# Kernel optimization log

Measured on AMD Instinct MI355X. Metric: run time of the kernel, lower is better.

## Reference

```python
import jax, jax.numpy as jnp
import numpy as np

N, E = 10000, 320000          # nodes, edges
NF, EF = 128, 64              # raw node / edge feat dims
HN, HE = 256, 256             # hidden node / edge dims
NO, EO = 128, 64              # decoder out dims
ITERS = 3


def _w(k, shape):
    # Linear/GRU weight init scaled by fan_in
    return jax.random.normal(k, shape, jnp.float32) / np.sqrt(shape[-1])


def setup_inputs() -> dict:
    key = jax.random.key(0)
    ks = jax.random.split(key, 12)
    return dict(
        nf=jax.random.normal(ks[0], (N, NF), jnp.float32),
        ef=jax.random.normal(ks[1], (E, EF), jnp.float32),
        src=jax.random.randint(ks[2], (E,), 0, N),
        dst=jax.random.randint(ks[3], (E,), 0, N),
        # encoders
        Wne=_w(ks[4], (HN, NF)), bne=jnp.zeros((HN,), jnp.float32),
        Wee=_w(ks[5], (HE, EF)), bee=jnp.zeros((HE,), jnp.float32),
        # edge GRUCell: input = concat(h_src, h_dst) -> 2*HN
        Wih_e=_w(ks[6], (3 * HE, 2 * HN)), Whh_e=_w(ks[7], (3 * HE, HE)),
        bih_e=jnp.zeros((3 * HE,), jnp.float32), bhh_e=jnp.zeros((3 * HE,), jnp.float32),
        # node GRUCell: input = aggregated edge messages -> HE
        Wih_n=_w(ks[8], (3 * HN, HE)), Whh_n=_w(ks[9], (3 * HN, HN)),
        bih_n=jnp.zeros((3 * HN,), jnp.float32), bhh_n=jnp.zeros((3 * HN,), jnp.float32),
        # decoders (MLP with num_neurons=[] == single Linear)
        Wnd=_w(ks[10], (NO, HN)), bnd=jnp.zeros((NO,), jnp.float32),
        Wed=_w(ks[11], (EO, HE)), bed=jnp.zeros((EO,), jnp.float32),
    )


def _gru(x, h, Wih, Whh, bih, bhh):
    # torch.nn.GRUCell math
    gi = x @ Wih.T + bih
    gh = h @ Whh.T + bhh
    ir, iz, inn = jnp.split(gi, 3, axis=-1)
    hr, hz, hn = jnp.split(gh, 3, axis=-1)
    r = jax.nn.sigmoid(ir + hr)
    z = jax.nn.sigmoid(iz + hz)
    n = jnp.tanh(inn + r * hn)
    return (1.0 - z) * n + z * h


def reference(nf, ef, src, dst, Wne, bne, Wee, bee,
              Wih_e, Whh_e, bih_e, bhh_e,
              Wih_n, Whh_n, bih_n, bhh_n,
              Wnd, bnd, Wed, bed):
    # encode
    unf = nf @ Wne.T + bne   # [N, HN]
    uef = ef @ Wee.T + bee   # [E, HE]
    # GRUMPNN: iterative GRU-based message passing
    for _ in range(ITERS):
        xe = jnp.concatenate([unf[src], unf[dst]], axis=-1)      # [E, 2*HN]
        uef = _gru(xe, uef, Wih_e, Whh_e, bih_e, bhh_e)           # edge update
        agg = jax.ops.segment_sum(uef, dst, num_segments=N)       # [N, HE]
        unf = _gru(agg, unf, Wih_n, Whh_n, bih_n, bhh_n)          # node update
    # decode
    return unf @ Wnd.T + bnd, uef @ Wed.T + bed
```

## Files before the change

### kernel.cpp

```cpp
#include <hip/hip_runtime.h>
#include <hip/hip_bf16.h>
#include <cstddef>

typedef _Float16 f16;
typedef f16 f16x8 __attribute__((ext_vector_type(8)));
typedef f16 f16x4 __attribute__((ext_vector_type(4)));
typedef f16 f16x16 __attribute__((ext_vector_type(16)));
typedef float f32x4 __attribute__((ext_vector_type(4)));

#define NNODES 10000
#define NEDGES 320000

__global__ void pack_b(const float* __restrict__ W, f16* __restrict__ P,
                       int Nout, int K, int ldw, int k0) {
    int idx = blockIdx.x * 256 + threadIdx.x;
    int total = Nout * K;
    if (idx >= total) return;
    int i = idx & 7;
    int l = (idx >> 3) & 63;
    int rest = idx >> 9;
    int NB = Nout >> 4;
    int nb = rest % NB;
    int ks = rest / NB;
    int k = ks * 32 + ((l >> 4) << 3) + i;
    int n = nb * 16 + (l & 15);
    P[idx] = (f16)W[(size_t)n * ldw + k0 + k];
}

template <int AMODE, int OMODE>
__global__ void gemm_bias(const void* __restrict__ A_, const f16* __restrict__ P,
                          const float* __restrict__ bias, void* __restrict__ C_,
                          int M, int Nout, int K) {
    const int lane = threadIdx.x & 63, wave = threadIdx.x >> 6;
    const int wm = wave >> 1, wn = wave & 1;
    const int rb = blockIdx.x * 64 + wm * 32;
    const int cb = blockIdx.y * 64 + wn * 32;
    const int NB = Nout >> 4;
    const int kl = (lane >> 4) << 3;
    int r0 = rb + (lane & 15);
    int r1 = r0 + 16;
    int rc0 = r0 < M ? r0 : M - 1;
    int rc1 = r1 < M ? r1 : M - 1;
    f32x4 acc[2][2] = {};
    for (int ks = 0; ks < (K >> 5); ++ks) {
        int kb = ks * 32 + kl;
        f16x8 a0, a1;
        if constexpr (AMODE == 1) {
            const f16* A = (const f16*)A_;
            a0 = *(const f16x8*)(A + (size_t)rc0 * K + kb);
            a1 = *(const f16x8*)(A + (size_t)rc1 * K + kb);
        } else {
            const float* A = (const float*)A_;
            const float* p0 = A + (size_t)rc0 * K + kb;
            const float* p1 = A + (size_t)rc1 * K + kb;
#pragma unroll
            for (int i = 0; i < 8; ++i) { a0[i] = (f16)p0[i]; a1[i] = (f16)p1[i]; }
        }
#pragma unroll
        for (int nf = 0; nf < 2; ++nf) {
            int nb = (cb >> 4) + nf;
            f16x8 b = *(const f16x8*)(P + (((size_t)ks * NB + nb) * 64 + lane) * 8);
            acc[0][nf] = __builtin_amdgcn_mfma_f32_16x16x32_f16(a0, b, acc[0][nf], 0, 0, 0);
            acc[1][nf] = __builtin_amdgcn_mfma_f32_16x16x32_f16(a1, b, acc[1][nf], 0, 0, 0);
        }
    }
#pragma unroll
    for (int mf = 0; mf < 2; ++mf)
#pragma unroll
        for (int nf = 0; nf < 2; ++nf)
#pragma unroll
            for (int reg = 0; reg < 4; ++reg) {
                int row = rb + mf * 16 + ((lane >> 4) << 2) + reg;
                int col = cb + nf * 16 + (lane & 15);
                if (row < M) {
                    float v = acc[mf][nf][reg] + bias[col];
                    if constexpr (OMODE == 0)
                        ((float*)C_)[(size_t)row * Nout + col] = v;
                    else
                        ((f16*)C_)[(size_t)row * Nout + col] = (f16)v;
                }
            }
}

template <bool BIAS>
__global__ void gemm_gi(const f16* __restrict__ A, const f16* __restrict__ P,
                        const float* __restrict__ bias, f16* __restrict__ G, int M) {
    const int lane = threadIdx.x & 63, wave = threadIdx.x >> 6;
    const int wm = wave >> 1, wn = wave & 1;
    const int rb = blockIdx.x * 64 + wm * 32;
    const int cb = blockIdx.y * 64 + wn * 32;
    const int NB = 48;
    const int kl = (lane >> 4) << 3;
    int r0 = rb + (lane & 15);
    int r1 = r0 + 16;
    int rc0 = r0 < M ? r0 : M - 1;
    int rc1 = r1 < M ? r1 : M - 1;
    f32x4 acc[2][2] = {};
    for (int ks = 0; ks < 8; ++ks) {
        int kb = ks * 32 + kl;
        f16x8 a0 = *(const f16x8*)(A + (size_t)rc0 * 256 + kb);
        f16x8 a1 = *(const f16x8*)(A + (size_t)rc1 * 256 + kb);
#pragma unroll
        for (int nf = 0; nf < 2; ++nf) {
            int nb = (cb >> 4) + nf;
            f16x8 b = *(const f16x8*)(P + (((size_t)ks * NB + nb) * 64 + lane) * 8);
            acc[0][nf] = __builtin_amdgcn_mfma_f32_16x16x32_f16(a0, b, acc[0][nf], 0, 0, 0);
            acc[1][nf] = __builtin_amdgcn_mfma_f32_16x16x32_f16(a1, b, acc[1][nf], 0, 0, 0);
        }
    }
#pragma unroll
    for (int mf = 0; mf < 2; ++mf)
#pragma unroll
        for (int nf = 0; nf < 2; ++nf)
#pragma unroll
            for (int reg = 0; reg < 4; ++reg) {
                int row = rb + mf * 16 + ((lane >> 4) << 2) + reg;
                int col = cb + nf * 16 + (lane & 15);
                if (row < M) {
                    float v = acc[mf][nf][reg];
                    if constexpr (BIAS) v += bias[col];
                    G[(size_t)row * 1024 + (col & 255) * 4 + (col >> 8)] = (f16)v;
                }
            }
}

__device__ inline float sigmoidf_(float x) {
    return __fdividef(1.f, 1.f + __expf(-x));
}
__device__ inline float tanhf_(float x) {
    float t = __expf(2.f * x);
    return 1.f - __fdividef(2.f, t + 1.f);
}

__global__ __launch_bounds__(1024, 4) void edge_gru(
        const f16* __restrict__ Gs, const f16* __restrict__ Gd,
        f16* __restrict__ uef,
        const int* __restrict__ src, const int* __restrict__ dst,
        const f16* __restrict__ Phh, const float* __restrict__ bhh) {
    __shared__ int s_idx[128];
    __shared__ char lds_h[64 * 528];
    const int t = threadIdx.x;
    const int e0 = blockIdx.x * 64;
    if (t < 64) s_idx[t] = src[e0 + t];
    else if (t < 128) s_idx[t] = dst[e0 + t - 64];
#pragma unroll
    for (int i = 0; i < 2; ++i) {
        int s = t + i * 1024;
        int row = s >> 5, seg = s & 31;
        f16x8 v = *(const f16x8*)(uef + (size_t)(e0 + row) * 256 + seg * 8);
        *(f16x8*)(lds_h + row * 528 + seg * 16) = v;
    }
    __syncthreads();
    const int lane = t & 63;
    const int wv = t >> 6;
    const int klb = (lane >> 4) << 4;
    const int erow = lane & 15;
    f32x4 acc[3][4] = {};
#pragma unroll
    for (int ks = 0; ks < 8; ++ks) {
        f16x8 b[4];
#pragma unroll
        for (int eg = 0; eg < 4; ++eg)
            b[eg] = *(const f16x8*)(lds_h + (eg * 16 + erow) * 528 + ks * 64 + klb);
#pragma unroll
        for (int g = 0; g < 3; ++g) {
            f16x8 a = *(const f16x8*)(Phh + (size_t)g * 65536
                                      + (((size_t)ks * 16 + wv) * 64 + lane) * 8);
#pragma unroll
            for (int eg = 0; eg < 4; ++eg)
                acc[g][eg] = __builtin_amdgcn_mfma_f32_16x16x32_f16(a, b[eg], acc[g][eg], 0, 0, 0);
        }
    }
    __syncthreads();
    {
        const int j0 = wv * 16 + ((lane >> 4) << 2);
        const f32x4 bhr = *(const f32x4*)(bhh + j0);
        const f32x4 bhz = *(const f32x4*)(bhh + 256 + j0);
        const f32x4 bhn = *(const f32x4*)(bhh + 512 + j0);
#pragma unroll
        for (int eg = 0; eg < 4; ++eg) {
            const int rr = eg * 16 + erow;
            const int sn = s_idx[rr], dn = s_idx[64 + rr];
            f16x16 gsv = *(const f16x16*)(Gs + (size_t)sn * 1024 + j0 * 4);
            f16x16 gdv = *(const f16x16*)(Gd + (size_t)dn * 1024 + j0 * 4);
            f16x4 hv = *(const f16x4*)(lds_h + rr * 528 + j0 * 2);
            f16x4 outv;
#pragma unroll
            for (int q = 0; q < 4; ++q) {
                float ir = (float)gsv[q * 4 + 0] + (float)gdv[q * 4 + 0];
                float iz = (float)gsv[q * 4 + 1] + (float)gdv[q * 4 + 1];
                float in = (float)gsv[q * 4 + 2] + (float)gdv[q * 4 + 2];
                float r = sigmoidf_(ir + acc[0][eg][q] + bhr[q]);
                float z = sigmoidf_(iz + acc[1][eg][q] + bhz[q]);
                float nn = tanhf_(in + r * (acc[2][eg][q] + bhn[q]));
                float h = (float)hv[q];
                outv[q] = (f16)(nn + z * (h - nn));
            }
            *(f16x4*)(lds_h + rr * 528 + j0 * 2) = outv;
        }
    }
    __syncthreads();
#pragma unroll
    for (int i = 0; i < 2; ++i) {
        int s = t + i * 1024;
        int row = s >> 5, seg = s & 31;
        f16x8 v = *(const f16x8*)(lds_h + row * 528 + seg * 16);
        *(f16x8*)(uef + (size_t)(e0 + row) * 256 + seg * 8) = v;
    }
}

__global__ __launch_bounds__(1024) void node_gru(
        const float* __restrict__ agg, f16* __restrict__ unf16,
        const f16* __restrict__ Pih, const f16* __restrict__ Phh,
        const float* __restrict__ bih, const float* __restrict__ bhh, int M) {
    const int lane = threadIdx.x & 63, wave = threadIdx.x >> 6;
    const int wm = wave & 1, wn = wave >> 1;
    const int rb = blockIdx.x * 64 + wm * 32;
    const int cb = wn * 32;
    const int nb0 = wn * 2;
    const int kl = (lane >> 4) << 3;
    int r0 = rb + (lane & 15), r1 = r0 + 16;
    int rc0 = r0 < M ? r0 : M - 1;
    int rc1 = r1 < M ? r1 : M - 1;
    f32x4 acc[4][2][2] = {};
#pragma unroll
    for (int ks = 0; ks < 8; ++ks) {
        const float* p0 = agg + (size_t)rc0 * 256 + ks * 32 + kl;
        const float* p1 = agg + (size_t)rc1 * 256 + ks * 32 + kl;
        f16x8 a0, a1;
#pragma unroll
        for (int i = 0; i < 8; ++i) { a0[i] = (f16)p0[i]; a1[i] = (f16)p1[i]; }
#pragma unroll
        for (int g = 0; g < 3; ++g) {
            const f16* Pg = Pih + (size_t)g * (256 * 256);
#pragma unroll
            for (int nf = 0; nf < 2; ++nf) {
                f16x8 b = *(const f16x8*)(Pg + (((size_t)ks * 16 + nb0 + nf) * 64 + lane) * 8);
                acc[g][0][nf] = __builtin_amdgcn_mfma_f32_16x16x32_f16(a0, b, acc[g][0][nf], 0, 0, 0);
                acc[g][1][nf] = __builtin_amdgcn_mfma_f32_16x16x32_f16(a1, b, acc[g][1][nf], 0, 0, 0);
            }
        }
    }
#pragma unroll
    for (int ks = 0; ks < 8; ++ks) {
        f16x8 a0 = *(const f16x8*)(unf16 + (size_t)rc0 * 256 + ks * 32 + kl);
        f16x8 a1 = *(const f16x8*)(unf16 + (size_t)rc1 * 256 + ks * 32 + kl);
#pragma unroll
        for (int g = 0; g < 3; ++g) {
            const f16* Pg = Phh + (size_t)g * (256 * 256);
            const int tgt = (g == 2) ? 3 : g;
#pragma unroll
            for (int nf = 0; nf < 2; ++nf) {
                f16x8 b = *(const f16x8*)(Pg + (((size_t)ks * 16 + nb0 + nf) * 64 + lane) * 8);
                acc[tgt][0][nf] = __builtin_amdgcn_mfma_f32_16x16x32_f16(a0, b, acc[tgt][0][nf], 0, 0, 0);
                acc[tgt][1][nf] = __builtin_amdgcn_mfma_f32_16x16x32_f16(a1, b, acc[tgt][1][nf], 0, 0, 0);
            }
        }
    }
    __syncthreads();
#pragma unroll
    for (int mf = 0; mf < 2; ++mf) {
        const int row = rb + mf * 16 + ((lane >> 4) << 2);
#pragma unroll
        for (int nf = 0; nf < 2; ++nf) {
            const int j = cb + nf * 16 + (lane & 15);
            const float b_r = bih[j] + bhh[j];
            const float b_z = bih[256 + j] + bhh[256 + j];
            const float b_i = bih[512 + j];
            const float b_h = bhh[512 + j];
#pragma unroll
            for (int reg = 0; reg < 4; ++reg) {
                const int rr = row + reg;
                if (rr < M) {
                    float r = sigmoidf_(acc[0][mf][nf][reg] + b_r);
                    float z = sigmoidf_(acc[1][mf][nf][reg] + b_z);
                    float nn = tanhf_(acc[2][mf][nf][reg] + b_i + r * (acc[3][mf][nf][reg] + b_h));
                    float h = (float)unf16[(size_t)rr * 256 + j];
                    unf16[(size_t)rr * 256 + j] = (f16)(nn + z * (h - nn));
                }
            }
        }
    }
}

__global__ void hist_k(const int* __restrict__ dst, int* __restrict__ cnt, int E) {
    int e = blockIdx.x * 256 + threadIdx.x;
    if (e < E) atomicAdd(&cnt[dst[e]], 1);
}

__global__ void scan_k(const int* __restrict__ cnt, int* __restrict__ rowptr, int n) {
    __shared__ int s[1024];
    __shared__ int carry_s;
    if (threadIdx.x == 0) { carry_s = 0; rowptr[0] = 0; }
    __syncthreads();
    for (int base = 0; base < n; base += 1024) {
        int i = base + (int)threadIdx.x;
        int v = (i < n) ? cnt[i] : 0;
        s[threadIdx.x] = v;
        __syncthreads();
        for (int off = 1; off < 1024; off <<= 1) {
            int tv = (threadIdx.x >= (unsigned)off) ? s[threadIdx.x - off] : 0;
            __syncthreads();
            s[threadIdx.x] += tv;
            __syncthreads();
        }
        if (i < n) rowptr[i + 1] = carry_s + s[threadIdx.x];
        __syncthreads();
        if (threadIdx.x == 0) carry_s += s[1023];
        __syncthreads();
    }
}

__global__ void scatter_k(const int* __restrict__ dst, const int* __restrict__ rowptr,
                          int* __restrict__ cnt2, int* __restrict__ eidx, int E) {
    int e = blockIdx.x * 256 + threadIdx.x;
    if (e < E) {
        int d = dst[e];
        int p = rowptr[d] + atomicAdd(&cnt2[d], 1);
        eidx[p] = e;
    }
}

__global__ void aggregate_k(const f16* __restrict__ uef, const int* __restrict__ eidx,
                            const int* __restrict__ rowptr, float* __restrict__ agg) {
    const int n = blockIdx.x;
    const int c = threadIdx.x;
    const int b = rowptr[n], e = rowptr[n + 1];
    float acc = 0.f;
    for (int j = b; j < e; ++j) acc += (float)uef[(size_t)eidx[j] * 256 + c];
    agg[(size_t)n * 256 + c] = acc;
}

extern "C" void kernel_launch(void* const* d_in, const int* in_sizes, int n_in,
                              void* d_out, int out_size, void* d_ws, size_t ws_size,
                              hipStream_t stream) {
    (void)in_sizes; (void)n_in; (void)out_size; (void)ws_size;
    const float* nf    = (const float*)d_in[0];
    const float* ef    = (const float*)d_in[1];
    const int*   src   = (const int*)d_in[2];
    const int*   dst   = (const int*)d_in[3];
    const float* Wne   = (const float*)d_in[4];
    const float* bne   = (const float*)d_in[5];
    const float* Wee   = (const float*)d_in[6];
    const float* bee   = (const float*)d_in[7];
    const float* Wih_e = (const float*)d_in[8];
    const float* Whh_e = (const float*)d_in[9];
    const float* bih_e = (const float*)d_in[10];
    const float* bhh_e = (const float*)d_in[11];
    const float* Wih_n = (const float*)d_in[12];
    const float* Whh_n = (const float*)d_in[13];
    const float* bih_n = (const float*)d_in[14];
    const float* bhh_n = (const float*)d_in[15];
    const float* Wnd   = (const float*)d_in[16];
    const float* bnd   = (const float*)d_in[17];
    const float* Wed   = (const float*)d_in[18];
    const float* bed   = (const float*)d_in[19];

    char* ws = (char*)d_ws;
    size_t off = 0;
    auto alloc = [&](size_t bytes) -> void* {
        void* p = ws + off;
        off += (bytes + 255) & ~(size_t)255;
        return p;
    };
    f16*   uefA  = (f16*)alloc((size_t)NEDGES * 256 * 2);
    f16*   unf16 = (f16*)alloc((size_t)NNODES * 256 * 2);
    float* agg   = (float*)alloc((size_t)NNODES * 256 * 4);
    f16*   Gs    = (f16*)alloc((size_t)NNODES * 1024 * 2);
    f16*   Gd    = (f16*)alloc((size_t)NNODES * 1024 * 2);
    f16*   Ps_e  = (f16*)alloc((size_t)768 * 256 * 2);
    f16*   Pd_e  = (f16*)alloc((size_t)768 * 256 * 2);
    f16*   Phh_e = (f16*)alloc((size_t)3 * 256 * 256 * 2);
    f16*   Pih_n = (f16*)alloc((size_t)3 * 256 * 256 * 2);
    f16*   Phh_n = (f16*)alloc((size_t)3 * 256 * 256 * 2);
    f16*   Pne   = (f16*)alloc((size_t)256 * 128 * 2);
    f16*   Pee   = (f16*)alloc((size_t)256 * 64 * 2);
    f16*   Pnd   = (f16*)alloc((size_t)128 * 256 * 2);
    f16*   Ped   = (f16*)alloc((size_t)64 * 256 * 2);
    int* cnt    = (int*)alloc((size_t)NNODES * 4);
    int* cnt2   = (int*)alloc((size_t)NNODES * 4);
    int* rowptr = (int*)alloc((size_t)(NNODES + 1) * 4);
    int* eidx   = (int*)alloc((size_t)NEDGES * 4);

    hipMemsetAsync(cnt, 0, (size_t)NNODES * 4, stream);
    hipMemsetAsync(cnt2, 0, (size_t)NNODES * 4, stream);

    pack_b<<<(768 * 256 + 255) / 256, 256, 0, stream>>>(Wih_e, Ps_e, 768, 256, 512, 0);
    pack_b<<<(768 * 256 + 255) / 256, 256, 0, stream>>>(Wih_e, Pd_e, 768, 256, 512, 256);
    for (int g = 0; g < 3; ++g) {
        pack_b<<<(256 * 256 + 255) / 256, 256, 0, stream>>>(Whh_e + (size_t)g * 256 * 256,
                                                            Phh_e + (size_t)g * 256 * 256, 256, 256, 256, 0);
        pack_b<<<(256 * 256 + 255) / 256, 256, 0, stream>>>(Wih_n + (size_t)g * 256 * 256,
                                                            Pih_n + (size_t)g * 256 * 256, 256, 256, 256, 0);
        pack_b<<<(256 * 256 + 255) / 256, 256, 0, stream>>>(Whh_n + (size_t)g * 256 * 256,
                                                            Phh_n + (size_t)g * 256 * 256, 256, 256, 256, 0);
    }
    pack_b<<<(256 * 128 + 255) / 256, 256, 0, stream>>>(Wne, Pne, 256, 128, 128, 0);
    pack_b<<<(256 * 64 + 255) / 256, 256, 0, stream>>>(Wee, Pee, 256, 64, 64, 0);
    pack_b<<<(128 * 256 + 255) / 256, 256, 0, stream>>>(Wnd, Pnd, 128, 256, 256, 0);
    pack_b<<<(64 * 256 + 255) / 256, 256, 0, stream>>>(Wed, Ped, 64, 256, 256, 0);

    hist_k<<<(NEDGES + 255) / 256, 256, 0, stream>>>(dst, cnt, NEDGES);
    scan_k<<<1, 1024, 0, stream>>>(cnt, rowptr, NNODES);
    scatter_k<<<(NEDGES + 255) / 256, 256, 0, stream>>>(dst, rowptr, cnt2, eidx, NEDGES);

    gemm_bias<0, 1><<<dim3(157, 4), 256, 0, stream>>>(nf, Pne, bne, unf16, NNODES, 256, 128);
    gemm_bias<0, 1><<<dim3(5000, 4), 256, 0, stream>>>(ef, Pee, bee, uefA, NEDGES, 256, 64);

    for (int it = 0; it < 3; ++it) {
        gemm_gi<true ><<<dim3(157, 12), 256, 0, stream>>>(unf16, Ps_e, bih_e, Gs, NNODES);
        gemm_gi<false><<<dim3(157, 12), 256, 0, stream>>>(unf16, Pd_e, bih_e, Gd, NNODES);
        edge_gru<<<5000, 1024, 0, stream>>>(Gs, Gd, uefA, src, dst, Phh_e, bhh_e);
        aggregate_k<<<NNODES, 256, 0, stream>>>(uefA, eidx, rowptr, agg);
        node_gru<<<157, 1024, 0, stream>>>(agg, unf16, Pih_n, Phh_n, bih_n, bhh_n, NNODES);
    }

    gemm_bias<1, 0><<<dim3(157, 2), 256, 0, stream>>>(unf16, Pnd, bnd, d_out, NNODES, 128, 256);
    gemm_bias<1, 0><<<dim3(5000, 1), 256, 0, stream>>>(uefA, Ped, bed,
                                                       (float*)d_out + (size_t)NNODES * 128,
                                                       NEDGES, 64, 256);
}
```

Measured before the change: 1.863 ms.

## Fuse segment-sum into edge GRU via dst-sorted edge order and atomics

The edge GRU kernel now walks edges in dst-sorted order through eidx, gathering and scattering uef rows by edge id. After the update it reduces runs of consecutive same-dst rows in LDS and atomically adds them into a zeroed agg buffer, which removes the separate aggregate kernel and its second read of uef. The two gi GEMM launches are also merged into one grid. The cost is indirect, less coalesced uef access, float atomics whose order is nondeterministic, and an extra memset each iteration.

```diff
diff --git a/kernel.cpp b/kernel.cpp
--- a/kernel.cpp
+++ b/kernel.cpp
@@ -82,13 +82,19 @@
             }
 }
 
-template <bool BIAS>
-__global__ void gemm_gi(const f16* __restrict__ A, const f16* __restrict__ P,
-                        const float* __restrict__ bias, f16* __restrict__ G, int M) {
+__global__ void gemm_gi2(const f16* __restrict__ A,
+                         const f16* __restrict__ Ps, const f16* __restrict__ Pd,
+                         const float* __restrict__ bias,
+                         f16* __restrict__ Gs, f16* __restrict__ Gd, int M) {
+    const int by = blockIdx.y;
+    const bool isD = by >= 12;
+    const f16* P = isD ? Pd : Ps;
+    f16* G = isD ? Gd : Gs;
+    const int byy = isD ? by - 12 : by;
     const int lane = threadIdx.x & 63, wave = threadIdx.x >> 6;
     const int wm = wave >> 1, wn = wave & 1;
     const int rb = blockIdx.x * 64 + wm * 32;
-    const int cb = blockIdx.y * 64 + wn * 32;
+    const int cb = byy * 64 + wn * 32;
     const int NB = 48;
     const int kl = (lane >> 4) << 3;
     int r0 = rb + (lane & 15);
@@ -118,7 +124,7 @@
                 int col = cb + nf * 16 + (lane & 15);
                 if (row < M) {
                     float v = acc[mf][nf][reg];
-                    if constexpr (BIAS) v += bias[col];
+                    if (!isD) v += bias[col];
                     G[(size_t)row * 1024 + (col & 255) * 4 + (col >> 8)] = (f16)v;
                 }
             }
@@ -136,18 +142,27 @@
         const f16* __restrict__ Gs, const f16* __restrict__ Gd,
         f16* __restrict__ uef,
         const int* __restrict__ src, const int* __restrict__ dst,
-        const f16* __restrict__ Phh, const float* __restrict__ bhh) {
-    __shared__ int s_idx[128];
+        const int* __restrict__ eidx,
+        const f16* __restrict__ Phh, const float* __restrict__ bhh,
+        float* __restrict__ agg) {
+    __shared__ int s_eid[64];
+    __shared__ int s_src[64];
+    __shared__ int s_dst[64];
     __shared__ char lds_h[64 * 528];
     const int t = threadIdx.x;
-    const int e0 = blockIdx.x * 64;
-    if (t < 64) s_idx[t] = src[e0 + t];
-    else if (t < 128) s_idx[t] = dst[e0 + t - 64];
+    const int p0 = blockIdx.x * 64;
+    if (t < 64) {
+        int e = eidx[p0 + t];
+        s_eid[t] = e;
+        s_src[t] = src[e];
+        s_dst[t] = dst[e];
+    }
 #pragma unroll
     for (int i = 0; i < 2; ++i) {
         int s = t + i * 1024;
         int row = s >> 5, seg = s & 31;
-        f16x8 v = *(const f16x8*)(uef + (size_t)(e0 + row) * 256 + seg * 8);
+        int e = eidx[p0 + row];
+        f16x8 v = *(const f16x8*)(uef + (size_t)e * 256 + seg * 8);
         *(f16x8*)(lds_h + row * 528 + seg * 16) = v;
     }
     __syncthreads();
@@ -180,7 +195,7 @@
 #pragma unroll
         for (int eg = 0; eg < 4; ++eg) {
             const int rr = eg * 16 + erow;
-            const int sn = s_idx[rr], dn = s_idx[64 + rr];
+            const int sn = s_src[rr], dn = s_dst[rr];
             f16x16 gsv = *(const f16x16*)(Gs + (size_t)sn * 1024 + j0 * 4);
             f16x16 gdv = *(const f16x16*)(Gd + (size_t)dn * 1024 + j0 * 4);
             f16x4 hv = *(const f16x4*)(lds_h + rr * 528 + j0 * 2);
@@ -205,7 +220,23 @@
         int s = t + i * 1024;
         int row = s >> 5, seg = s & 31;
         f16x8 v = *(const f16x8*)(lds_h + row * 528 + seg * 16);
-        *(f16x8*)(uef + (size_t)(e0 + row) * 256 + seg * 8) = v;
+        *(f16x8*)(uef + (size_t)s_eid[row] * 256 + seg * 8) = v;
+    }
+    {
+        const int c = t & 255;
+        const int q = t >> 8;
+        float a = 0.f;
+        int d = s_dst[q * 16];
+#pragma unroll
+        for (int r = q * 16; r < q * 16 + 16; ++r) {
+            a += (float)*(const f16*)(lds_h + r * 528 + c * 2);
+            int dn = (r < 63) ? s_dst[r + 1] : -1;
+            if (r == q * 16 + 15 || dn != d) {
+                atomicAdd(&agg[(size_t)d * 256 + c], a);
+                a = 0.f;
+                d = dn;
+            }
+        }
     }
 }
 
@@ -319,16 +350,6 @@
         int p = rowptr[d] + atomicAdd(&cnt2[d], 1);
         eidx[p] = e;
     }
-}
-
-__global__ void aggregate_k(const f16* __restrict__ uef, const int* __restrict__ eidx,
-                            const int* __restrict__ rowptr, float* __restrict__ agg) {
-    const int n = blockIdx.x;
-    const int c = threadIdx.x;
-    const int b = rowptr[n], e = rowptr[n + 1];
-    float acc = 0.f;
-    for (int j = b; j < e; ++j) acc += (float)uef[(size_t)eidx[j] * 256 + c];
-    agg[(size_t)n * 256 + c] = acc;
 }
 
 extern "C" void kernel_launch(void* const* d_in, const int* in_sizes, int n_in,
@@ -408,10 +429,9 @@
     gemm_bias<0, 1><<<dim3(5000, 4), 256, 0, stream>>>(ef, Pee, bee, uefA, NEDGES, 256, 64);
 
     for (int it = 0; it < 3; ++it) {
-        gemm_gi<true ><<<dim3(157, 12), 256, 0, stream>>>(unf16, Ps_e, bih_e, Gs, NNODES);
-        gemm_gi<false><<<dim3(157, 12), 256, 0, stream>>>(unf16, Pd_e, bih_e, Gd, NNODES);
-        edge_gru<<<5000, 1024, 0, stream>>>(Gs, Gd, uefA, src, dst, Phh_e, bhh_e);
-        aggregate_k<<<NNODES, 256, 0, stream>>>(uefA, eidx, rowptr, agg);
+        gemm_gi2<<<dim3(157, 24), 256, 0, stream>>>(unf16, Ps_e, Pd_e, bih_e, Gs, Gd, NNODES);
+        hipMemsetAsync(agg, 0, (size_t)NNODES * 256 * 4, stream);
+        edge_gru<<<5000, 1024, 0, stream>>>(Gs, Gd, uefA, src, dst, eidx, Phh_e, bhh_e, agg);
         node_gru<<<157, 1024, 0, stream>>>(agg, unf16, Pih_n, Phh_n, bih_n, bhh_n, NNODES);
     }
 
```

After: 1.752 ms. -6.0%, faster.
